# Performance work log

Measured on AMD Instinct MI355X. Metric: run time of the kernel, lower is better.

Reference implementation:

```python
import jax, jax.numpy as jnp
import numpy as np

B, IN, OUT = 512, 1024, 1024

def setup_inputs() -> dict:
    key = jax.random.key(0)
    kx, kw = jax.random.split(key)
    X = jax.random.normal(kx, (B, IN), dtype=jnp.float32)
    W = jax.random.normal(kw, (OUT, IN), dtype=jnp.float32) * 0.02  # init_std=0.02
    return {"X": X, "W": W}

def reference(X, W):
    # Tropical (max-plus) matmul: Y[b, j] = max_i (X[b, i] + W[j, i]).
    # leaky_factor=1 / is_random=False -> plain hard max in forward.
    # [B, 1, IN] + [1, OUT, IN] -> max over IN -> [B, OUT]
    return jnp.max(X[:, None, :] + W[None, :, :], axis=-1)
```

## Files before the change

### kernel.cpp

```cpp
#include <hip/hip_runtime.h>
#include <stdint.h>


#define M_DIM 512
#define N_DIM 1024
#define K_DIM 1024
#define CAP 128

#define OFF_WT    0
#define OFF_PMAX  (4u * 1024u * 1024u)
#define OFF_PMIN  (OFF_PMAX + 64u * 1024u)

__global__ __launch_bounds__(256)
void transpose_spread(const float* __restrict__ W, float* __restrict__ Wt,
                      float* __restrict__ pmax, float* __restrict__ pmin) {
    __shared__ float L[64][65];
    __shared__ float smx[4][64];
    __shared__ float smn[4][64];

    const int tid = threadIdx.x;
    const int kt = blockIdx.x;
    const int jt = blockIdx.y;
    const int k0 = kt * 64, j0 = jt * 64;

    {
        const int r = tid >> 2, q = tid & 3;
        const float* g = &W[(size_t)(j0 + r) * K_DIM + k0 + q * 16];
#pragma unroll
        for (int t = 0; t < 4; t++) {
            float4 f = *(const float4*)(g + 4 * t);
            L[r][q * 16 + 4 * t + 0] = f.x;
            L[r][q * 16 + 4 * t + 1] = f.y;
            L[r][q * 16 + 4 * t + 2] = f.z;
            L[r][q * 16 + 4 * t + 3] = f.w;
        }
    }
    __syncthreads();

    {
        const int kk = tid >> 2, q = tid & 3;
        float* o = &Wt[(size_t)(k0 + kk) * N_DIM + j0 + q * 16];
#pragma unroll
        for (int t = 0; t < 4; t++) {
            float4 f = {L[q * 16 + 4 * t + 0][kk], L[q * 16 + 4 * t + 1][kk],
                        L[q * 16 + 4 * t + 2][kk], L[q * 16 + 4 * t + 3][kk]};
            *(float4*)(o + 4 * t) = f;
        }
    }

    {
        const int jl = tid & 63, seg = tid >> 6;
        float mx = -3.0e38f, mn = 3.0e38f;
#pragma unroll
        for (int i = 0; i < 16; i++) {
            float v = L[jl][seg * 16 + i];
            mx = fmaxf(mx, v);
            mn = fminf(mn, v);
        }
        smx[seg][jl] = mx;
        smn[seg][jl] = mn;
    }
    __syncthreads();
    if (tid < 64) {
        float mx = fmaxf(fmaxf(smx[0][tid], smx[1][tid]), fmaxf(smx[2][tid], smx[3][tid]));
        float mn = fminf(fminf(smn[0][tid], smn[1][tid]), fminf(smn[2][tid], smn[3][tid]));
        pmax[kt * N_DIM + j0 + tid] = mx;
        pmin[kt * N_DIM + j0 + tid] = mn;
    }
}

__global__ __launch_bounds__(256)
void emit_pruned(const float* __restrict__ X, const float* __restrict__ Wt,
                 const float* __restrict__ pmax, const float* __restrict__ pmin,
                 float* __restrict__ out) {
    __shared__ float red[256];
    __shared__ float sval[CAP];
    __shared__ int sidx[CAP];
    __shared__ int scnt;

    const int tid = threadIdx.x;
    const int b = blockIdx.x;

    {
        float4 mx = {-3.0e38f, -3.0e38f, -3.0e38f, -3.0e38f};
        float4 mn = {3.0e38f, 3.0e38f, 3.0e38f, 3.0e38f};
#pragma unroll
        for (int kt = 0; kt < 16; kt++) {
            float4 a = ((const float4*)pmax)[kt * 256 + tid];
            float4 i = ((const float4*)pmin)[kt * 256 + tid];
            mx.x = fmaxf(mx.x, a.x); mx.y = fmaxf(mx.y, a.y);
            mx.z = fmaxf(mx.z, a.z); mx.w = fmaxf(mx.w, a.w);
            mn.x = fminf(mn.x, i.x); mn.y = fminf(mn.y, i.y);
            mn.z = fminf(mn.z, i.z); mn.w = fminf(mn.w, i.w);
        }
        float s0 = fmaxf(mx.x - mn.x, mx.y - mn.y);
        float s1 = fmaxf(mx.z - mn.z, mx.w - mn.w);
        red[tid] = fmaxf(s0, s1);
    }
    if (tid == 0) scnt = 0;
    __syncthreads();
    for (int s = 128; s > 0; s >>= 1) {
        if (tid < s) red[tid] = fmaxf(red[tid], red[tid + s]);
        __syncthreads();
    }
    const float D = red[0] * 1.0001f + 1e-6f;
    __syncthreads();

    const float4 xv = ((const float4*)X)[b * (K_DIM / 4) + tid];
    red[tid] = fmaxf(fmaxf(xv.x, xv.y), fmaxf(xv.z, xv.w));
    __syncthreads();
    for (int s = 128; s > 0; s >>= 1) {
        if (tid < s) red[tid] = fmaxf(red[tid], red[tid + s]);
        __syncthreads();
    }
    const float thr = red[0] - D;

    const float xa[4] = {xv.x, xv.y, xv.z, xv.w};
#pragma unroll
    for (int c = 0; c < 4; c++) {
        if (xa[c] > thr) {
            int p = atomicAdd(&scnt, 1);
            if (p < CAP) { sidx[p] = tid * 4 + c; sval[p] = xa[c]; }
        }
    }
    __syncthreads();
    const int n = scnt;

    float4 acc = {-3.0e38f, -3.0e38f, -3.0e38f, -3.0e38f};
    if (n <= CAP) {
        for (int c = 0; c < n; c++) {
            const int k = sidx[c];
            const float xk = sval[c];
            const float4 w = ((const float4*)Wt)[k * (N_DIM / 4) + tid];
            acc.x = fmaxf(acc.x, xk + w.x);
            acc.y = fmaxf(acc.y, xk + w.y);
            acc.z = fmaxf(acc.z, xk + w.z);
            acc.w = fmaxf(acc.w, xk + w.w);
        }
    } else {
        for (int k = 0; k < K_DIM; k++) {
            const float xk = X[(size_t)b * K_DIM + k];
            const float4 w = ((const float4*)Wt)[k * (N_DIM / 4) + tid];
            acc.x = fmaxf(acc.x, xk + w.x);
            acc.y = fmaxf(acc.y, xk + w.y);
            acc.z = fmaxf(acc.z, xk + w.z);
            acc.w = fmaxf(acc.w, xk + w.w);
        }
    }
    ((float4*)out)[b * (N_DIM / 4) + tid] = acc;
}

extern "C" void kernel_launch(void* const* d_in, const int* in_sizes, int n_in,
                              void* d_out, int out_size, void* d_ws, size_t ws_size,
                              hipStream_t stream) {
    const float* X = (const float*)d_in[0];
    const float* W = (const float*)d_in[1];
    float* out = (float*)d_out;

    char* ws = (char*)d_ws;
    float* Wt   = (float*)(ws + OFF_WT);
    float* pmax = (float*)(ws + OFF_PMAX);
    float* pmin = (float*)(ws + OFF_PMIN);

    transpose_spread<<<dim3(K_DIM / 64, N_DIM / 64), 256, 0, stream>>>(W, Wt, pmax, pmin);
    emit_pruned<<<M_DIM, 256, 0, stream>>>(X, Wt, pmax, pmin, out);
}
```

Before: 66.69 us.

## Fuse transpose and pruned max-plus pass into one cooperative kernel

Merges the transpose/spread kernel and the pruned emission kernel into a single cooperative launch of 256 blocks, using grid-wide syncs to separate the phases. The global spread reduction D is now computed once, spread across blocks with a partial buffer, rather than every one of 512 blocks re-reading all pmax/pmin. Each block then handles two batch rows. This removes a kernel launch boundary and redundant reduction work, but adds two grid barriers and halves the block count for the main phase.

```diff
diff --git a/kernel.cpp b/kernel.cpp
--- a/kernel.cpp
+++ b/kernel.cpp
@@ -1,5 +1,8 @@
 #include <hip/hip_runtime.h>
+#include <hip/hip_cooperative_groups.h>
 #include <stdint.h>
+
+namespace cg = cooperative_groups;
 
 
 #define M_DIM 512
@@ -10,17 +13,27 @@
 #define OFF_WT    0
 #define OFF_PMAX  (4u * 1024u * 1024u)
 #define OFF_PMIN  (OFF_PMAX + 64u * 1024u)
+#define OFF_DPART (OFF_PMIN + 64u * 1024u)
 
 __global__ __launch_bounds__(256)
-void transpose_spread(const float* __restrict__ W, float* __restrict__ Wt,
-                      float* __restrict__ pmax, float* __restrict__ pmin) {
+void tropical_fused(const float* __restrict__ X, const float* __restrict__ W,
+                    float* __restrict__ out, float* __restrict__ Wt,
+                    float* __restrict__ pmax, float* __restrict__ pmin,
+                    float* __restrict__ Dpart) {
     __shared__ float L[64][65];
     __shared__ float smx[4][64];
     __shared__ float smn[4][64];
+    __shared__ float red[256];
+    __shared__ float sval[CAP];
+    __shared__ int sidx[CAP];
+    __shared__ int scnt;
+
+    cg::grid_group grid = cg::this_grid();
 
     const int tid = threadIdx.x;
-    const int kt = blockIdx.x;
-    const int jt = blockIdx.y;
+    const int bx = blockIdx.x;
+    const int kt = bx & 15;
+    const int jt = bx >> 4;
     const int k0 = kt * 64, j0 = jt * 64;
 
     {
@@ -36,7 +49,6 @@
         }
     }
     __syncthreads();
-
     {
         const int kk = tid >> 2, q = tid & 3;
         float* o = &Wt[(size_t)(k0 + kk) * N_DIM + j0 + q * 16];
@@ -47,7 +59,6 @@
             *(float4*)(o + 4 * t) = f;
         }
     }
-
     {
         const int jl = tid & 63, seg = tid >> 6;
         float mx = -3.0e38f, mn = 3.0e38f;
@@ -67,87 +78,93 @@
         pmax[kt * N_DIM + j0 + tid] = mx;
         pmin[kt * N_DIM + j0 + tid] = mn;
     }
-}
 
-__global__ __launch_bounds__(256)
-void emit_pruned(const float* __restrict__ X, const float* __restrict__ Wt,
-                 const float* __restrict__ pmax, const float* __restrict__ pmin,
-                 float* __restrict__ out) {
-    __shared__ float red[256];
-    __shared__ float sval[CAP];
-    __shared__ int sidx[CAP];
-    __shared__ int scnt;
-
-    const int tid = threadIdx.x;
-    const int b = blockIdx.x;
+    grid.sync();
 
     {
-        float4 mx = {-3.0e38f, -3.0e38f, -3.0e38f, -3.0e38f};
-        float4 mn = {3.0e38f, 3.0e38f, 3.0e38f, 3.0e38f};
+        if (tid < 64) {
+            const int j = bx * 4 + (tid >> 4);
+            const int ktt = tid & 15;
+            smx[0][tid] = pmax[ktt * N_DIM + j];
+            smn[0][tid] = pmin[ktt * N_DIM + j];
+        }
+        __syncthreads();
+        if (tid < 4) {
+            float mx = -3.0e38f, mn = 3.0e38f;
 #pragma unroll
-        for (int kt = 0; kt < 16; kt++) {
-            float4 a = ((const float4*)pmax)[kt * 256 + tid];
-            float4 i = ((const float4*)pmin)[kt * 256 + tid];
-            mx.x = fmaxf(mx.x, a.x); mx.y = fmaxf(mx.y, a.y);
-            mx.z = fmaxf(mx.z, a.z); mx.w = fmaxf(mx.w, a.w);
-            mn.x = fminf(mn.x, i.x); mn.y = fminf(mn.y, i.y);
-            mn.z = fminf(mn.z, i.z); mn.w = fminf(mn.w, i.w);
+            for (int ktt = 0; ktt < 16; ktt++) {
+                mx = fmaxf(mx, smx[0][tid * 16 + ktt]);
+                mn = fminf(mn, smn[0][tid * 16 + ktt]);
+            }
+            red[tid] = mx - mn;
         }
-        float s0 = fmaxf(mx.x - mn.x, mx.y - mn.y);
-        float s1 = fmaxf(mx.z - mn.z, mx.w - mn.w);
-        red[tid] = fmaxf(s0, s1);
+        __syncthreads();
+        if (tid == 0)
+            Dpart[bx] = fmaxf(fmaxf(red[0], red[1]), fmaxf(red[2], red[3]));
     }
-    if (tid == 0) scnt = 0;
+
+    grid.sync();
+
+    if (tid < 64) {
+        float4 dp = ((const float4*)Dpart)[tid];
+        red[tid] = fmaxf(fmaxf(dp.x, dp.y), fmaxf(dp.z, dp.w));
+    }
     __syncthreads();
-    for (int s = 128; s > 0; s >>= 1) {
+    for (int s = 32; s > 0; s >>= 1) {
         if (tid < s) red[tid] = fmaxf(red[tid], red[tid + s]);
         __syncthreads();
     }
     const float D = red[0] * 1.0001f + 1e-6f;
-    __syncthreads();
 
-    const float4 xv = ((const float4*)X)[b * (K_DIM / 4) + tid];
-    red[tid] = fmaxf(fmaxf(xv.x, xv.y), fmaxf(xv.z, xv.w));
-    __syncthreads();
-    for (int s = 128; s > 0; s >>= 1) {
-        if (tid < s) red[tid] = fmaxf(red[tid], red[tid + s]);
+#pragma unroll 1
+    for (int rep = 0; rep < 2; rep++) {
+        const int b = bx * 2 + rep;
+
         __syncthreads();
+        const float4 xv = ((const float4*)X)[b * (K_DIM / 4) + tid];
+        red[tid] = fmaxf(fmaxf(xv.x, xv.y), fmaxf(xv.z, xv.w));
+        if (tid == 0) scnt = 0;
+        __syncthreads();
+        for (int s = 128; s > 0; s >>= 1) {
+            if (tid < s) red[tid] = fmaxf(red[tid], red[tid + s]);
+            __syncthreads();
+        }
+        const float thr = red[0] - D;
+
+        const float xa[4] = {xv.x, xv.y, xv.z, xv.w};
+#pragma unroll
+        for (int c = 0; c < 4; c++) {
+            if (xa[c] > thr) {
+                int p = atomicAdd(&scnt, 1);
+                if (p < CAP) { sidx[p] = tid * 4 + c; sval[p] = xa[c]; }
+            }
+        }
+        __syncthreads();
+        const int n = scnt;
+
+        float4 acc = {-3.0e38f, -3.0e38f, -3.0e38f, -3.0e38f};
+        if (n <= CAP) {
+            for (int c = 0; c < n; c++) {
+                const int k = sidx[c];
+                const float xk = sval[c];
+                const float4 w = ((const float4*)Wt)[k * (N_DIM / 4) + tid];
+                acc.x = fmaxf(acc.x, xk + w.x);
+                acc.y = fmaxf(acc.y, xk + w.y);
+                acc.z = fmaxf(acc.z, xk + w.z);
+                acc.w = fmaxf(acc.w, xk + w.w);
+            }
+        } else {
+            for (int k = 0; k < K_DIM; k++) {
+                const float xk = X[(size_t)b * K_DIM + k];
+                const float4 w = ((const float4*)Wt)[k * (N_DIM / 4) + tid];
+                acc.x = fmaxf(acc.x, xk + w.x);
+                acc.y = fmaxf(acc.y, xk + w.y);
+                acc.z = fmaxf(acc.z, xk + w.z);
+                acc.w = fmaxf(acc.w, xk + w.w);
+            }
+        }
+        ((float4*)out)[b * (N_DIM / 4) + tid] = acc;
     }
-    const float thr = red[0] - D;
-
-    const float xa[4] = {xv.x, xv.y, xv.z, xv.w};
-#pragma unroll
-    for (int c = 0; c < 4; c++) {
-        if (xa[c] > thr) {
-            int p = atomicAdd(&scnt, 1);
-            if (p < CAP) { sidx[p] = tid * 4 + c; sval[p] = xa[c]; }
-        }
-    }
-    __syncthreads();
-    const int n = scnt;
-
-    float4 acc = {-3.0e38f, -3.0e38f, -3.0e38f, -3.0e38f};
-    if (n <= CAP) {
-        for (int c = 0; c < n; c++) {
-            const int k = sidx[c];
-            const float xk = sval[c];
-            const float4 w = ((const float4*)Wt)[k * (N_DIM / 4) + tid];
-            acc.x = fmaxf(acc.x, xk + w.x);
-            acc.y = fmaxf(acc.y, xk + w.y);
-            acc.z = fmaxf(acc.z, xk + w.z);
-            acc.w = fmaxf(acc.w, xk + w.w);
-        }
-    } else {
-        for (int k = 0; k < K_DIM; k++) {
-            const float xk = X[(size_t)b * K_DIM + k];
-            const float4 w = ((const float4*)Wt)[k * (N_DIM / 4) + tid];
-            acc.x = fmaxf(acc.x, xk + w.x);
-            acc.y = fmaxf(acc.y, xk + w.y);
-            acc.z = fmaxf(acc.z, xk + w.z);
-            acc.w = fmaxf(acc.w, xk + w.w);
-        }
-    }
-    ((float4*)out)[b * (N_DIM / 4) + tid] = acc;
 }
 
 extern "C" void kernel_launch(void* const* d_in, const int* in_sizes, int n_in,
@@ -158,10 +175,13 @@
     float* out = (float*)d_out;
 
     char* ws = (char*)d_ws;
-    float* Wt   = (float*)(ws + OFF_WT);
-    float* pmax = (float*)(ws + OFF_PMAX);
-    float* pmin = (float*)(ws + OFF_PMIN);
+    float* Wt    = (float*)(ws + OFF_WT);
+    float* pmax  = (float*)(ws + OFF_PMAX);
+    float* pmin  = (float*)(ws + OFF_PMIN);
+    float* Dpart = (float*)(ws + OFF_DPART);
 
-    transpose_spread<<<dim3(K_DIM / 64, N_DIM / 64), 256, 0, stream>>>(W, Wt, pmax, pmin);
-    emit_pruned<<<M_DIM, 256, 0, stream>>>(X, Wt, pmax, pmin, out);
+    void* args[] = {(void*)&X, (void*)&W, (void*)&out, (void*)&Wt,
+                    (void*)&pmax, (void*)&pmin, (void*)&Dpart};
+    hipLaunchCooperativeKernel((const void*)tropical_fused,
+                               dim3(256), dim3(256), args, 0, stream);
 }
```

New measurement: 133.1 us. 2x slower.
